# Optimization experiments

Measured on AMD Instinct MI355X. Metric: run time of the kernel, lower is better.

Reference implementation:

```python
import jax, jax.numpy as jnp
import numpy as np

N_NODES = 100000
N_EDGES = 3200000
D_IN = 256
D_HID = 256
N_CLS = 8


def spmm(row, col, val, x):
    # sparse [N,N] @ dense [N,F]: gather neighbor rows, scale, segment-sum by dest row
    msgs = val[:, None] * x[col]  # [E, F]
    return jax.ops.segment_sum(msgs, row, num_segments=N_NODES)


def setup_inputs() -> dict:
    key = jax.random.key(0)
    ks = jax.random.split(key, 8)
    x = jax.random.normal(ks[0], (N_NODES, D_IN), dtype=jnp.float32)
    adj_row = jax.random.randint(ks[1], (N_EDGES,), 0, N_NODES, dtype=jnp.int32)
    adj_col = jax.random.randint(ks[2], (N_EDGES,), 0, N_NODES, dtype=jnp.int32)
    adj_val = jax.random.uniform(ks[3], (N_EDGES,), dtype=jnp.float32)
    W1 = jax.random.normal(ks[4], (D_IN, D_HID), dtype=jnp.float32) / np.sqrt(D_IN)
    b1 = jnp.zeros((D_HID,), dtype=jnp.float32)
    W2 = jax.random.normal(ks[5], (D_HID, N_CLS), dtype=jnp.float32) / np.sqrt(D_HID)
    b2 = jnp.zeros((N_CLS,), dtype=jnp.float32)
    return {"x": x, "adj_row": adj_row, "adj_col": adj_col, "adj_val": adj_val,
            "W1": W1, "b1": b1, "W2": W2, "b2": b2}


def reference(x, adj_row, adj_col, adj_val, W1, b1, W2, b2):
    h = spmm(adj_row, adj_col, adj_val, x)            # [N, D_IN]
    h = jax.nn.relu(h @ W1 + b1)                      # [N, D_HID]
    h = spmm(adj_row, adj_col, adj_val, h)            # [N, D_HID]
    logits = h @ W2 + b2                              # [N, N_CLS]
    return jax.nn.log_softmax(logits, axis=1)
```

## Files before the change

kernel.cpp:

```cpp
#include <hip/hip_runtime.h>
#include <hip/hip_bf16.h>


constexpr int N_NODES = 100000;
constexpr int N_EDGES = 3200000;
constexpr int D = 256;
constexpr int NCLS = 8;

constexpr int NBUCK  = 391;
constexpr int BCHUNK = 6400;
constexpr int EPT    = BCHUNK / 256;

constexpr int CVT_BLOCKS  = N_NODES / 4;
constexpr int CNT_BLOCKS  = N_EDGES / BCHUNK;
constexpr int PACK_BLOCKS = D * D / 256;

typedef __attribute__((ext_vector_type(8))) short bf16x8;
typedef __attribute__((ext_vector_type(4))) float f32x4;

__device__ inline unsigned short f2bf(float f) {
    __hip_bfloat16 h = __float2bfloat16(f);
    return __builtin_bit_cast(unsigned short, h);
}


__global__ __launch_bounds__(256) void prep_kernel(const float* __restrict__ x,
                                                   unsigned char* __restrict__ x8,
                                                   float* __restrict__ scl,
                                                   const int* __restrict__ row,
                                                   int* __restrict__ bucket_cnt,
                                                   const float* __restrict__ W1,
                                                   unsigned short* __restrict__ w1p,
                                                   const float* __restrict__ W2,
                                                   unsigned short* __restrict__ w2p) {
    const int bid = blockIdx.x;
    if (bid < CVT_BLOCKS) {
        const int wave = threadIdx.x >> 6;
        const int lane = threadIdx.x & 63;
        const int r = bid * 4 + wave;
        const float4 v = ((const float4*)x)[r * 64 + lane];
        float am = fmaxf(fmaxf(fabsf(v.x), fabsf(v.y)), fmaxf(fabsf(v.z), fabsf(v.w)));
        #pragma unroll
        for (int o = 32; o > 0; o >>= 1) am = fmaxf(am, __shfl_xor(am, o));
        const float inv = (am > 0.f) ? 127.f / am : 0.f;
        const int q0 = (int)rintf(v.x * inv);
        const int q1 = (int)rintf(v.y * inv);
        const int q2 = (int)rintf(v.z * inv);
        const int q3 = (int)rintf(v.w * inv);
        const unsigned pk = (unsigned)(q0 & 255) | ((unsigned)(q1 & 255) << 8) |
                            ((unsigned)(q2 & 255) << 16) | ((unsigned)(q3 & 255) << 24);
        ((unsigned*)x8)[r * 64 + lane] = pk;
        if (lane == 0) scl[r] = am * (1.f / 127.f);
    } else if (bid < CVT_BLOCKS + CNT_BLOCKS) {
        __shared__ int h[NBUCK];
        for (int i = threadIdx.x; i < NBUCK; i += 256) h[i] = 0;
        __syncthreads();
        const int base = (bid - CVT_BLOCKS) * BCHUNK + threadIdx.x;
        #pragma unroll
        for (int j = 0; j < EPT; j++) atomicAdd(&h[row[base + j * 256] >> 8], 1);
        __syncthreads();
        for (int i = threadIdx.x; i < NBUCK; i += 256)
            if (h[i]) atomicAdd(&bucket_cnt[i], h[i]);
    } else if (bid < CVT_BLOCKS + CNT_BLOCKS + PACK_BLOCKS) {
        int idx = (bid - CVT_BLOCKS - CNT_BLOCKS) * 256 + threadIdx.x;
        int j = idx & 7, lane = (idx >> 3) & 63, s = (idx >> 9) & 7, nt = idx >> 12;
        int k = s * 32 + (lane >> 4) * 8 + j;
        int n = nt * 16 + (lane & 15);
        w1p[idx] = f2bf(W1[k * D + n]);
    } else {
        for (int i = threadIdx.x; i < 8 * 64 * 8; i += 256) {
            int j = i & 7, lane = (i >> 3) & 63, s = i >> 9;
            int k = s * 32 + ((lane >> 4)) * 8 + j;
            int n = lane & 15;
            w2p[i] = (n < NCLS) ? f2bf(W2[k * NCLS + n]) : (unsigned short)0;
        }
    }
}


__global__ __launch_bounds__(256) void bucket_scan_kernel(const int* __restrict__ bucket_cnt,
                                                          int* __restrict__ bucket_base,
                                                          int* __restrict__ bucket_next) {
    __shared__ int h[512];
    const int t = threadIdx.x;
    int c0 = (t < NBUCK) ? bucket_cnt[t] : 0;
    int c1 = (t + 256 < NBUCK) ? bucket_cnt[t + 256] : 0;
    h[t] = c0; h[t + 256] = c1;
    __syncthreads();
    for (int o = 1; o < 512; o <<= 1) {
        int v0 = (t >= o) ? h[t - o] : 0;
        int v1 = (t + 256 >= o) ? h[t + 256 - o] : 0;
        __syncthreads();
        h[t] += v0; h[t + 256] += v1;
        __syncthreads();
    }
    if (t < NBUCK)        { int e = h[t] - c0;        bucket_base[t] = e;        bucket_next[t] = e; }
    if (t + 256 < NBUCK)  { int e = h[t + 256] - c1;  bucket_base[t + 256] = e;  bucket_next[t + 256] = e; }
    if (t == 0) bucket_base[NBUCK] = h[511];
}


__global__ __launch_bounds__(256) void bin_scatter_kernel(const int* __restrict__ row,
                                                          const int* __restrict__ col,
                                                          const float* __restrict__ val,
                                                          int* __restrict__ bucket_next,
                                                          int* __restrict__ bcv) {
    __shared__ int s_cv[BCHUNK];
    __shared__ unsigned short s_bk[BCHUNK];
    __shared__ int s_h[512];
    __shared__ int s_base[512];
    __shared__ int s_cur[NBUCK];
    const int t = threadIdx.x;
    const int base = blockIdx.x * BCHUNK + t;

    int rl[EPT]; int cvl[EPT];
    #pragma unroll
    for (int j = 0; j < EPT; j++) {
        int i = base + j * 256;
        int r = row[i];
        rl[j] = r;
        unsigned q = (unsigned)__builtin_fminf(val[i] * 128.f + 0.5f, 127.f);
        cvl[j] = col[i] | ((r & 255) << 17) | (int)(q << 25);
    }
    s_h[t] = 0; s_h[t + 256] = 0;
    __syncthreads();
    #pragma unroll
    for (int j = 0; j < EPT; j++) atomicAdd(&s_h[rl[j] >> 8], 1);
    __syncthreads();
    int c0 = s_h[t], c1 = s_h[t + 256];
    for (int o = 1; o < 512; o <<= 1) {
        int v0 = (t >= o) ? s_h[t - o] : 0;
        int v1 = (t + 256 >= o) ? s_h[t + 256 - o] : 0;
        __syncthreads();
        s_h[t] += v0; s_h[t + 256] += v1;
        __syncthreads();
    }
    const int e0 = s_h[t] - c0;
    const int e1 = s_h[t + 256] - c1;
    if (t < NBUCK) s_cur[t] = e0;
    if (t + 256 < NBUCK) s_cur[t + 256] = e1;
    __syncthreads();
    #pragma unroll
    for (int j = 0; j < EPT; j++) {
        int b = rl[j] >> 8;
        int q = atomicAdd(&s_cur[b], 1);
        s_cv[q] = cvl[j];
        s_bk[q] = (unsigned short)b;
    }
    if (t < NBUCK)       s_base[t]       = (c0 > 0 ? atomicAdd(&bucket_next[t], c0)       : 0) - e0;
    if (t + 256 < NBUCK) s_base[t + 256] = (c1 > 0 ? atomicAdd(&bucket_next[t + 256], c1) : 0) - e1;
    __syncthreads();
    for (int i = t; i < BCHUNK; i += 256) {
        bcv[s_base[s_bk[i]] + i] = s_cv[i];
    }
}


__global__ __launch_bounds__(1024) void reorder_kernel(const int* __restrict__ bucket_base,
                                                       const int* __restrict__ bcv,
                                                       const float* __restrict__ scl,
                                                       int* __restrict__ offsets,
                                                       int* __restrict__ edges,
                                                       int* __restrict__ edgr) {
    __shared__ int rh[256];
    __shared__ int cur[256];
    const int b = blockIdx.x;
    const int t = threadIdx.x;
    const int base = bucket_base[b];
    const int cnt  = bucket_base[b + 1] - base;

    if (t < 256) rh[t] = 0;
    __syncthreads();
    for (int i = t; i < cnt; i += 1024) atomicAdd(&rh[((unsigned)bcv[base + i] >> 17) & 255], 1);
    __syncthreads();
    const int myc = (t < 256) ? rh[t] : 0;
    for (int o = 1; o < 256; o <<= 1) {
        int v = (t < 256 && t >= o) ? rh[t - o] : 0;
        __syncthreads();
        if (t < 256) rh[t] += v;
        __syncthreads();
    }
    if (t < 256) {
        const int excl = rh[t] - myc;
        const int grow = (b << 8) + t;
        if (grow <= N_NODES) offsets[grow] = base + excl;
        cur[t] = base + excl;
    }
    __syncthreads();
    for (int i = t; i < cnt; i += 1024) {
        const unsigned wrd = (unsigned)bcv[base + i];
        const int r8 = (wrd >> 17) & 255;
        const int c  = (int)(wrd & 0x1FFFFu);
        const int p = atomicAdd(&cur[r8], 1);
        const float f = (float)(wrd >> 25) * 0.0078125f;
        edgr[p] = (int)((__float_as_uint(f) & 0xFFFE0000u) | (unsigned)c);
        const float fs = f * scl[c];
        unsigned u = __float_as_uint(fs);
        u = (u + 0x00010000u) & 0xFFFE0000u;
        edges[p] = (int)(u | (unsigned)c);
    }
}


constexpr int SCPITCH = 264;

__global__ __launch_bounds__(256) void spmm_gemm_proj_kernel(const int* __restrict__ offs,
                                                             const int* __restrict__ edges,
                                                             const unsigned char* __restrict__ x8,
                                                             const unsigned short* __restrict__ w1p,
                                                             const float* __restrict__ b1,
                                                             const unsigned short* __restrict__ w2p,
                                                             float* __restrict__ g) {
    __shared__ unsigned short sC[32 * SCPITCH];

    const int tid  = threadIdx.x;
    const int wave = tid >> 6;
    const int lane = tid & 63;
    const int quad = lane >> 4;
    const int l15  = lane & 15;
    const int row0 = blockIdx.x * 32;

    int off_l = 0;
    if (lane < 9) off_l = offs[row0 + wave * 8 + lane];

    for (int idx = 0; idx < 8; idx++) {
        const int s = __builtin_amdgcn_readlane(off_l, idx);
        const int e = __builtin_amdgcn_readlane(off_l, idx + 1);
        float4 acc = make_float4(0.f, 0.f, 0.f, 0.f);

        for (int base = s; base < e; base += 64) {
            const int rem = e - base;
            int ed = 0;
            if (lane < rem) ed = edges[base + lane];
            const int cnt = rem < 64 ? rem : 64;
            for (int gb = 0; gb < cnt; gb += 8) {
                unsigned wv[8]; unsigned p[8];
                #pragma unroll
                for (int u = 0; u < 8; u++)
                    wv[u] = (unsigned)__builtin_amdgcn_readlane(ed, gb + u);
                #pragma unroll
                for (int u = 0; u < 8; u++) {
                    const size_t c = wv[u] & 0x1FFFFu;
                    p[u] = *((const unsigned*)(x8 + (c << 8)) + lane);
                }
                #pragma unroll
                for (int u = 0; u < 8; u++) {
                    const float v = __uint_as_float(wv[u] & 0xFFFE0000u);
                    const unsigned pk = p[u];
                    acc.x = fmaf(v, (float)((int)(pk << 24) >> 24), acc.x);
                    acc.y = fmaf(v, (float)((int)(pk << 16) >> 24), acc.y);
                    acc.z = fmaf(v, (float)((int)(pk <<  8) >> 24), acc.z);
                    acc.w = fmaf(v, (float)((int)pk >> 24),         acc.w);
                }
            }
        }
        const int rl = wave * 8 + idx;
        ushort4 o;
        o.x = f2bf(acc.x); o.y = f2bf(acc.y); o.z = f2bf(acc.z); o.w = f2bf(acc.w);
        *(ushort4*)&sC[rl * SCPITCH + lane * 4] = o;
    }
    __syncthreads();

    const int ntb = wave * 4;
    f32x4 acc[2][4] = {};

    #pragma unroll
    for (int s = 0; s < 8; s++) {
        bf16x8 a[2], b[4];
        #pragma unroll
        for (int mt = 0; mt < 2; mt++)
            a[mt] = __builtin_bit_cast(bf16x8,
                *(const uint4*)&sC[(mt * 16 + l15) * SCPITCH + s * 32 + quad * 8]);
        #pragma unroll
        for (int nt = 0; nt < 4; nt++)
            b[nt] = __builtin_bit_cast(bf16x8,
                *(const uint4*)(w1p + (((size_t)(ntb + nt) * 8 + s) * 64 + lane) * 8));
        #pragma unroll
        for (int mt = 0; mt < 2; mt++)
            #pragma unroll
            for (int nt = 0; nt < 4; nt++)
                acc[mt][nt] = __builtin_amdgcn_mfma_f32_16x16x32_bf16(a[mt], b[nt], acc[mt][nt], 0, 0, 0);
    }
    __syncthreads();

    #pragma unroll
    for (int nt = 0; nt < 4; nt++) {
        const int n = (ntb + nt) * 16 + l15;
        const float bias = b1[n];
        #pragma unroll
        for (int mt = 0; mt < 2; mt++) {
            #pragma unroll
            for (int i = 0; i < 4; i++) {
                const int rl = mt * 16 + quad * 4 + i;
                float v = acc[mt][nt][i] + bias;
                sC[rl * SCPITCH + n] = f2bf(v > 0.f ? v : 0.f);
            }
        }
    }
    __syncthreads();

    if (wave < 2) {
        f32x4 pacc = {};
        #pragma unroll
        for (int s = 0; s < 8; s++) {
            bf16x8 a = __builtin_bit_cast(bf16x8,
                *(const uint4*)&sC[(wave * 16 + l15) * SCPITCH + s * 32 + quad * 8]);
            bf16x8 b = __builtin_bit_cast(bf16x8,
                *(const uint4*)(w2p + ((size_t)s * 64 + lane) * 8));
            pacc = __builtin_amdgcn_mfma_f32_16x16x32_bf16(a, b, pacc, 0, 0, 0);
        }
        if (l15 < NCLS) {
            #pragma unroll
            for (int i = 0; i < 4; i++) {
                const int grow = row0 + wave * 16 + quad * 4 + i;
                g[(size_t)grow * NCLS + l15] = pacc[i];
            }
        }
    }
}


__global__ __launch_bounds__(256) void head_spmm_kernel(const int* __restrict__ offs,
                                                        const int* __restrict__ edgr,
                                                        const float* __restrict__ g,
                                                        const float* __restrict__ b2,
                                                        float* __restrict__ out) {
    const int tid  = threadIdx.x;
    const int hw   = tid >> 5;
    const int hl   = tid & 31;
    const int node = blockIdx.x * 8 + hw;
    if (node >= N_NODES) return;

    const int s = offs[node];
    const int e = offs[node + 1];

    float acc[NCLS] = {};
    for (int base = s; base < e; base += 32) {
        const int rem = e - base;
        if (hl < rem) {
            const unsigned w = (unsigned)edgr[base + hl];
            const int   c = (int)(w & 0x1FFFFu);
            const float v = __uint_as_float(w & 0xFFFE0000u);
            const float4* gp = (const float4*)(g + (size_t)c * NCLS);
            const float4 lo = gp[0];
            const float4 hi = gp[1];
            acc[0] = fmaf(v, lo.x, acc[0]); acc[1] = fmaf(v, lo.y, acc[1]);
            acc[2] = fmaf(v, lo.z, acc[2]); acc[3] = fmaf(v, lo.w, acc[3]);
            acc[4] = fmaf(v, hi.x, acc[4]); acc[5] = fmaf(v, hi.y, acc[5]);
            acc[6] = fmaf(v, hi.z, acc[6]); acc[7] = fmaf(v, hi.w, acc[7]);
        }
    }
    #pragma unroll
    for (int c = 0; c < NCLS; c++) {
        #pragma unroll
        for (int o = 16; o > 0; o >>= 1) acc[c] += __shfl_xor(acc[c], o);
    }

    float logits[NCLS];
    #pragma unroll
    for (int c = 0; c < NCLS; c++) logits[c] = acc[c] + b2[c];
    float m = logits[0];
    #pragma unroll
    for (int c = 1; c < NCLS; c++) m = fmaxf(m, logits[c]);
    float sum = 0.f;
    #pragma unroll
    for (int c = 0; c < NCLS; c++) sum += __expf(logits[c] - m);
    const float lse = m + __logf(sum);
    if (hl < NCLS) out[(size_t)node * NCLS + hl] = logits[hl] - lse;
}


extern "C" void kernel_launch(void* const* d_in, const int* in_sizes, int n_in,
                              void* d_out, int out_size, void* d_ws, size_t ws_size,
                              hipStream_t stream) {
    const float* x       = (const float*)d_in[0];
    const int*   adj_row = (const int*)  d_in[1];
    const int*   adj_col = (const int*)  d_in[2];
    const float* adj_val = (const float*)d_in[3];
    const float* W1      = (const float*)d_in[4];
    const float* b1      = (const float*)d_in[5];
    const float* W2      = (const float*)d_in[6];
    const float* b2      = (const float*)d_in[7];
    float* out = (float*)d_out;

    char* w = (char*)d_ws;
    auto alloc = [&](size_t bytes) -> char* {
        char* p = w;
        w += (bytes + 255) & ~(size_t)255;
        return p;
    };
    int*            bucket_cnt  = (int*)  alloc((NBUCK + 1) * 4);
    int*            bucket_base = (int*)  alloc((NBUCK + 1) * 4);
    int*            bucket_next = (int*)  alloc((NBUCK + 1) * 4);
    int*            offsets     = (int*)  alloc(((size_t)N_NODES + 1) * 4);
    int*            bcv         = (int*)  alloc((size_t)N_EDGES * 4);
    int*            edges       = (int*)  alloc((size_t)N_EDGES * 4);
    int*            edgr        = (int*)  alloc((size_t)N_EDGES * 4);
    unsigned char*  x8          = (unsigned char*)alloc((size_t)N_NODES * D);
    float*          scl         = (float*)alloc((size_t)N_NODES * 4);
    unsigned short* w1p         = (unsigned short*)alloc((size_t)D * D * 2);
    unsigned short* w2p         = (unsigned short*)alloc((size_t)8 * 64 * 8 * 2);
    float*          g           = (float*)alloc((size_t)N_NODES * NCLS * 4);

    hipMemsetAsync(bucket_cnt, 0, (NBUCK + 1) * 4, stream);

    prep_kernel<<<CVT_BLOCKS + CNT_BLOCKS + PACK_BLOCKS + 1, 256, 0, stream>>>(
        x, x8, scl, adj_row, bucket_cnt, W1, w1p, W2, w2p);

    bucket_scan_kernel<<<1, 256, 0, stream>>>(bucket_cnt, bucket_base, bucket_next);

    bin_scatter_kernel<<<N_EDGES / BCHUNK, 256, 0, stream>>>(
        adj_row, adj_col, adj_val, bucket_next, bcv);

    reorder_kernel<<<NBUCK, 1024, 0, stream>>>(bucket_base, bcv, scl, offsets, edges, edgr);

    spmm_gemm_proj_kernel<<<N_NODES / 32, 256, 0, stream>>>(
        offsets, edges, x8, w1p, b1, w2p, g);

    const int nb8 = (N_NODES + 7) / 8;
    head_spmm_kernel<<<nb8, 256, 0, stream>>>(offsets, edgr, g, b2, out);
}
```

Baseline: 422.4 us.

## Reuse scaled edge array in head SpMM and store projected logits as bf16

Drops the separate edgr array, which held unscaled edge values. The head SpMM now reads the scaled edges array and cancels the per-node scale by dividing the projected logits by scl before storing them. The projected logits g are written as bf16 (16 bytes per node instead of 32), so the random gather in the head SpMM moves half the bytes and the reorder kernel saves a 12.8MB write. In exchange it costs extra bf16 rounding, and the scale is clamped to avoid dividing by zero.

```diff
diff --git a/kernel.cpp b/kernel.cpp
--- a/kernel.cpp
+++ b/kernel.cpp
@@ -22,6 +22,8 @@
     __hip_bfloat16 h = __float2bfloat16(f);
     return __builtin_bit_cast(unsigned short, h);
 }
+__device__ inline float bflo(unsigned u) { return __uint_as_float(u << 16); }
+__device__ inline float bfhi(unsigned u) { return __uint_as_float(u & 0xffff0000u); }
 
 
 __global__ __launch_bounds__(256) void prep_kernel(const float* __restrict__ x,
@@ -42,7 +44,8 @@
         float am = fmaxf(fmaxf(fabsf(v.x), fabsf(v.y)), fmaxf(fabsf(v.z), fabsf(v.w)));
         #pragma unroll
         for (int o = 32; o > 0; o >>= 1) am = fmaxf(am, __shfl_xor(am, o));
-        const float inv = (am > 0.f) ? 127.f / am : 0.f;
+        am = fmaxf(am, 1e-5f);
+        const float inv = 127.f / am;
         const int q0 = (int)rintf(v.x * inv);
         const int q1 = (int)rintf(v.y * inv);
         const int q2 = (int)rintf(v.z * inv);
@@ -160,8 +163,7 @@
                                                        const int* __restrict__ bcv,
                                                        const float* __restrict__ scl,
                                                        int* __restrict__ offsets,
-                                                       int* __restrict__ edges,
-                                                       int* __restrict__ edgr) {
+                                                       int* __restrict__ edges) {
     __shared__ int rh[256];
     __shared__ int cur[256];
     const int b = blockIdx.x;
@@ -193,7 +195,6 @@
         const int c  = (int)(wrd & 0x1FFFFu);
         const int p = atomicAdd(&cur[r8], 1);
         const float f = (float)(wrd >> 25) * 0.0078125f;
-        edgr[p] = (int)((__float_as_uint(f) & 0xFFFE0000u) | (unsigned)c);
         const float fs = f * scl[c];
         unsigned u = __float_as_uint(fs);
         u = (u + 0x00010000u) & 0xFFFE0000u;
@@ -210,7 +211,8 @@
                                                              const unsigned short* __restrict__ w1p,
                                                              const float* __restrict__ b1,
                                                              const unsigned short* __restrict__ w2p,
-                                                             float* __restrict__ g) {
+                                                             const float* __restrict__ scl,
+                                                             unsigned short* __restrict__ g2) {
     __shared__ unsigned short sC[32 * SCPITCH];
 
     const int tid  = threadIdx.x;
@@ -313,7 +315,8 @@
             #pragma unroll
             for (int i = 0; i < 4; i++) {
                 const int grow = row0 + wave * 16 + quad * 4 + i;
-                g[(size_t)grow * NCLS + l15] = pacc[i];
+                const float sv = scl[grow];
+                g2[(size_t)grow * NCLS + l15] = f2bf(pacc[i] / sv);
             }
         }
     }
@@ -321,8 +324,8 @@
 
 
 __global__ __launch_bounds__(256) void head_spmm_kernel(const int* __restrict__ offs,
-                                                        const int* __restrict__ edgr,
-                                                        const float* __restrict__ g,
+                                                        const int* __restrict__ edges,
+                                                        const unsigned short* __restrict__ g2,
                                                         const float* __restrict__ b2,
                                                         float* __restrict__ out) {
     const int tid  = threadIdx.x;
@@ -338,16 +341,14 @@
     for (int base = s; base < e; base += 32) {
         const int rem = e - base;
         if (hl < rem) {
-            const unsigned w = (unsigned)edgr[base + hl];
+            const unsigned w = (unsigned)edges[base + hl];
             const int   c = (int)(w & 0x1FFFFu);
             const float v = __uint_as_float(w & 0xFFFE0000u);
-            const float4* gp = (const float4*)(g + (size_t)c * NCLS);
-            const float4 lo = gp[0];
-            const float4 hi = gp[1];
-            acc[0] = fmaf(v, lo.x, acc[0]); acc[1] = fmaf(v, lo.y, acc[1]);
-            acc[2] = fmaf(v, lo.z, acc[2]); acc[3] = fmaf(v, lo.w, acc[3]);
-            acc[4] = fmaf(v, hi.x, acc[4]); acc[5] = fmaf(v, hi.y, acc[5]);
-            acc[6] = fmaf(v, hi.z, acc[6]); acc[7] = fmaf(v, hi.w, acc[7]);
+            const uint4 q = *((const uint4*)g2 + c);
+            acc[0] = fmaf(v, bflo(q.x), acc[0]); acc[1] = fmaf(v, bfhi(q.x), acc[1]);
+            acc[2] = fmaf(v, bflo(q.y), acc[2]); acc[3] = fmaf(v, bfhi(q.y), acc[3]);
+            acc[4] = fmaf(v, bflo(q.z), acc[4]); acc[5] = fmaf(v, bfhi(q.z), acc[5]);
+            acc[6] = fmaf(v, bflo(q.w), acc[6]); acc[7] = fmaf(v, bfhi(q.w), acc[7]);
         }
     }
     #pragma unroll
@@ -395,12 +396,11 @@
     int*            offsets     = (int*)  alloc(((size_t)N_NODES + 1) * 4);
     int*            bcv         = (int*)  alloc((size_t)N_EDGES * 4);
     int*            edges       = (int*)  alloc((size_t)N_EDGES * 4);
-    int*            edgr        = (int*)  alloc((size_t)N_EDGES * 4);
     unsigned char*  x8          = (unsigned char*)alloc((size_t)N_NODES * D);
     float*          scl         = (float*)alloc((size_t)N_NODES * 4);
     unsigned short* w1p         = (unsigned short*)alloc((size_t)D * D * 2);
     unsigned short* w2p         = (unsigned short*)alloc((size_t)8 * 64 * 8 * 2);
-    float*          g           = (float*)alloc((size_t)N_NODES * NCLS * 4);
+    unsigned short* g2          = (unsigned short*)alloc((size_t)N_NODES * NCLS * 2);
 
     hipMemsetAsync(bucket_cnt, 0, (NBUCK + 1) * 4, stream);
 
@@ -412,11 +412,11 @@
     bin_scatter_kernel<<<N_EDGES / BCHUNK, 256, 0, stream>>>(
         adj_row, adj_col, adj_val, bucket_next, bcv);
 
-    reorder_kernel<<<NBUCK, 1024, 0, stream>>>(bucket_base, bcv, scl, offsets, edges, edgr);
+    reorder_kernel<<<NBUCK, 1024, 0, stream>>>(bucket_base, bcv, scl, offsets, edges);
 
     spmm_gemm_proj_kernel<<<N_NODES / 32, 256, 0, stream>>>(
-        offsets, edges, x8, w1p, b1, w2p, g);
+        offsets, edges, x8, w1p, b1, w2p, scl, g2);
 
     const int nb8 = (N_NODES + 7) / 8;
-    head_spmm_kernel<<<nb8, 256, 0, stream>>>(offsets, edgr, g, b2, out);
-}
+    head_spmm_kernel<<<nb8, 256, 0, stream>>>(offsets, edges, g2, b2, out);
+}
```

New measurement: 404.3 us. 1.04x faster.
